# Kernel optimization log

Hardware: AMD Instinct MI355X
Metric: run time of the kernel (lower is better)

The kernel has to match this reference:

```python
import jax, jax.numpy as jnp
import numpy as np

N_MODELS = 16
IN_F = 1024
OUT_F = 1024
N_TOK = 8192


def setup_inputs() -> dict:
    key = jax.random.key(0)
    k1, k2, k3, k4 = jax.random.split(key, 4)
    x = jax.random.normal(k1, (N_TOK, IN_F), dtype=jnp.float32)
    idxs = jax.random.randint(k2, (N_TOK,), 0, N_MODELS, dtype=jnp.int64)
    w = jax.random.normal(k3, (N_MODELS, IN_F, OUT_F), dtype=jnp.float32) * 0.02
    b = jax.random.normal(k4, (N_MODELS, OUT_F), dtype=jnp.float32) * 0.02
    return {"x": x, "idxs": idxs, "w": w, "b": b}


def reference(x, idxs, w, b):
    # Equivalent math to the torch loop: for each expert i, tokens with
    # idxs==i get x @ w[i] + b[i]; finally ReLU over all outputs.
    # Loop over the small fixed expert count; selection by mask avoids
    # materializing the [N, E, out] tensor or gathering per-token weights.
    y = jnp.zeros((x.shape[0], w.shape[2]), dtype=x.dtype)
    for i in range(w.shape[0]):
        yi = x @ w[i] + b[i]  # [N, out]
        y = jnp.where((idxs == i)[:, None], yi, y)
    return jax.nn.relu(y)
```

## Files before the change

### kernel.cpp

```cpp
#include <hip/hip_runtime.h>
#include <hip/hip_bf16.h>
#include <stdint.h>

#define N_MODELS 16
#define IN_F 1024
#define OUT_F 1024
#define N_TOK 8192
#define MAX_MT 80

typedef unsigned short u16;
using us4   = __attribute__((ext_vector_type(4))) unsigned short;
using s16x8 = __attribute__((ext_vector_type(8))) short;
using f32x4 = __attribute__((ext_vector_type(4))) float;

__device__ __forceinline__ u16 f2bf(float f) {
    union { float f; uint32_t u; } v;
    v.f = f;
    uint32_t u = v.u;
    u += 0x7fffu + ((u >> 16) & 1u);
    return (u16)(u >> 16);
}

__device__ __forceinline__ void gload16(const u16* g, u16* l) {
    __builtin_amdgcn_global_load_lds(
        (const __attribute__((address_space(1))) void*)g,
        (__attribute__((address_space(3))) void*)l, 16, 0, 0);
}

__global__ void hist_kernel(const int* __restrict__ idxs, int* __restrict__ ghist) {
    __shared__ int cnt[N_MODELS];
    int t = threadIdx.x;
    if (t < N_MODELS) cnt[t] = 0;
    __syncthreads();
    int i = blockIdx.x * 256 + t;
    atomicAdd(&cnt[idxs[i]], 1);
    __syncthreads();
    if (t < N_MODELS) atomicAdd(&ghist[t], cnt[t]);
}

__global__ void scan_kernel(const int* __restrict__ ghist,
                            int* __restrict__ offs, int* __restrict__ tile_off,
                            int* __restrict__ gcur) {
    if (threadIdx.x == 0) {
        int o = 0, to = 0;
        for (int e = 0; e < N_MODELS; ++e) {
            offs[e] = o; tile_off[e] = to; gcur[e] = o;
            to += (ghist[e] + 127) >> 7;
            o  += ghist[e];
        }
        offs[N_MODELS] = o; tile_off[N_MODELS] = to;
    }
}

__global__ void scatter_kernel(const int* __restrict__ idxs,
                               int* __restrict__ gcur, int* __restrict__ perm) {
    int i = blockIdx.x * 256 + threadIdx.x;
    int e = idxs[i];
    int p = atomicAdd(&gcur[e], 1);
    perm[p] = i;
}

__global__ __launch_bounds__(256)
void wprep_kernel(const float* __restrict__ w, u16* __restrict__ wT) {
    int bx  = blockIdx.x;
    int e   = bx >> 7;
    int nt  = (bx >> 4) & 7;
    int kb2 = bx & 15;
    const float* wp = w + (size_t)e * (IN_F * OUT_F) + (size_t)kb2 * 64 * OUT_F + nt * 128;
    u16* ob = wT + ((size_t)(e * 8 + nt) * 32 + kb2 * 2) * 4096;
    int n    = threadIdx.x & 127;
    int half = threadIdx.x >> 7;
#pragma unroll
    for (int i = 0; i < 4; ++i) {
        int ko = half + i * 2;
        s16x8 v;
#pragma unroll
        for (int j = 0; j < 8; ++j)
            v[j] = (short)f2bf(wp[(size_t)(ko * 8 + j) * OUT_F + n]);
        *(s16x8*)(ob + ((size_t)((ko >> 2) * 4 + (ko & 3)) * 128 + n) * 8) = v;
    }
}

__global__ __launch_bounds__(256)
void xprep_kernel(const float* __restrict__ x,
                  const int* __restrict__ perm, const int* __restrict__ offs,
                  const int* __restrict__ tile_off, u16* __restrict__ xg) {
    __shared__ u16 sh[4096];
    int t   = threadIdx.x;
    int bx2 = blockIdx.x;
    int mt  = bx2 >> 3;
    int kg  = bx2 & 7;
    int total = tile_off[N_MODELS];
    if (mt >= total) return;
    int e = 0;
    while (tile_off[e + 1] <= mt) ++e;
    int s0   = offs[e] + (mt - tile_off[e]) * 128;
    int sEnd = offs[e + 1];
    int r0   = t >> 3;
    int apos = t & 7;
    int toks[4];
#pragma unroll
    for (int i = 0; i < 4; ++i) {
        int r = r0 + i * 32;
        toks[i] = (s0 + r < sEnd) ? perm[s0 + r] : -1;
    }
    u16* outx = xg + (size_t)mt * 32 * 4096;
    for (int kb4 = 0; kb4 < 4; ++kb4) {
        int kb = kg * 4 + kb4;
#pragma unroll
        for (int i = 0; i < 4; ++i) {
            int r = r0 + i * 32;
            int k = kb * 32 + apos * 4;
            float4 v;
            if (toks[i] >= 0) v = *(const float4*)(x + (size_t)toks[i] * IN_F + k);
            else              v = make_float4(0.f, 0.f, 0.f, 0.f);
            us4 pk; pk.x = f2bf(v.x); pk.y = f2bf(v.y); pk.z = f2bf(v.z); pk.w = f2bf(v.w);
            *(us4*)(&sh[(apos >> 1) * 1024 + r * 8 + (apos & 1) * 4]) = pk;
        }
        __syncthreads();
#pragma unroll
        for (int i = 0; i < 2; ++i) {
            int c = t + i * 256;
            *(s16x8*)(outx + (size_t)kb * 4096 + c * 8) = *(const s16x8*)(&sh[c * 8]);
        }
        __syncthreads();
    }
}

__global__ __launch_bounds__(256)
void gemm_kernel(const u16* __restrict__ xg, const u16* __restrict__ wT,
                 const float* __restrict__ bias,
                 const int* __restrict__ perm, const int* __restrict__ offs,
                 const int* __restrict__ tile_off,
                 float* __restrict__ out)
{
    __shared__ u16 As[4096];
    __shared__ u16 Bs[4096];
    __shared__ int   permS[128];
    __shared__ float biasS[128];
    __shared__ int   toS[N_MODELS + 1];

    int t  = threadIdx.x;
    int bt = blockIdx.y;
    int nt = blockIdx.x;

    if (t <= N_MODELS) toS[t] = tile_off[t];
    __syncthreads();
    if (bt >= toS[N_MODELS]) return;

    int e = 0;
    while (toS[e + 1] <= bt) ++e;
    int s0   = offs[e] + (bt - toS[e]) * 128;
    int sEnd = offs[e + 1];
    int mValid = sEnd - s0; if (mValid > 128) mValid = 128;

    if (t < 128) {
        permS[t] = (s0 + t < sEnd) ? perm[s0 + t] : 0;
        biasS[t] = bias[(size_t)e * OUT_F + nt * 128 + t];
    }

    const u16* atile = xg + (size_t)bt * 32 * 4096;
    const u16* btile = wT + ((size_t)(e * 8 + nt) * 32) * 4096;

    int lane = t & 63;
    int wv   = t >> 6;
    int wm   = (wv >> 1) * 64;
    int wn   = (wv & 1) * 64;
    int m    = lane & 15;
    int q    = lane >> 4;

    f32x4 acc[4][4];
#pragma unroll
    for (int i = 0; i < 4; ++i)
#pragma unroll
        for (int j = 0; j < 4; ++j)
            acc[i][j] = (f32x4){0.f, 0.f, 0.f, 0.f};

    int c = wv * 2;

    for (int kb = 0; kb < 32; ++kb) {
        const u16* ga = atile + kb * 4096;
        const u16* gb = btile + kb * 4096;
        gload16(ga + (c    ) * 512 + lane * 8, &As[(c    ) * 512]);
        gload16(ga + (c + 1) * 512 + lane * 8, &As[(c + 1) * 512]);
        gload16(gb + (c    ) * 512 + lane * 8, &Bs[(c    ) * 512]);
        gload16(gb + (c + 1) * 512 + lane * 8, &Bs[(c + 1) * 512]);
        __syncthreads();

        s16x8 af[4], bf[4];
#pragma unroll
        for (int mt2 = 0; mt2 < 4; ++mt2)
            af[mt2] = *(const s16x8*)(&As[q * 1024 + (wm + mt2 * 16 + m) * 8]);
#pragma unroll
        for (int nt2 = 0; nt2 < 4; ++nt2)
            bf[nt2] = *(const s16x8*)(&Bs[q * 1024 + (wn + nt2 * 16 + m) * 8]);
#pragma unroll
        for (int mt2 = 0; mt2 < 4; ++mt2)
#pragma unroll
            for (int nt2 = 0; nt2 < 4; ++nt2)
                acc[mt2][nt2] = __builtin_amdgcn_mfma_f32_16x16x32_bf16(
                    af[mt2], bf[nt2], acc[mt2][nt2], 0, 0, 0);
        __syncthreads();
    }

#pragma unroll
    for (int mt2 = 0; mt2 < 4; ++mt2) {
        int rbase = wm + mt2 * 16 + q * 4;
#pragma unroll
        for (int i = 0; i < 4; ++i) {
            int r = rbase + i;
            if (r < mValid) {
                int tok = permS[r];
                float* orow = out + (size_t)tok * OUT_F + nt * 128;
#pragma unroll
                for (int nt2 = 0; nt2 < 4; ++nt2) {
                    int col = wn + nt2 * 16 + m;
                    float v = acc[mt2][nt2][i] + biasS[col];
                    orow[col] = v > 0.f ? v : 0.f;
                }
            }
        }
    }
}

extern "C" void kernel_launch(void* const* d_in, const int* in_sizes, int n_in,
                              void* d_out, int out_size, void* d_ws, size_t ws_size,
                              hipStream_t stream) {
    const float* x    = (const float*)d_in[0];
    const int*   idxs = (const int*)d_in[1];
    const float* w    = (const float*)d_in[2];
    const float* b    = (const float*)d_in[3];
    float* out = (float*)d_out;

    u16* wT = (u16*)d_ws;
    u16* xg = wT + (size_t)N_MODELS * IN_F * OUT_F;
    int* perm     = (int*)(xg + (size_t)MAX_MT * 32 * 4096);
    int* offs     = perm + N_TOK;
    int* tile_off = offs + (N_MODELS + 1);
    int* ghist    = tile_off + (N_MODELS + 1);
    int* gcur     = ghist + N_MODELS;

    hipMemsetAsync(ghist, 0, N_MODELS * sizeof(int), stream);
    hist_kernel<<<N_TOK / 256, 256, 0, stream>>>(idxs, ghist);
    scan_kernel<<<1, 64, 0, stream>>>(ghist, offs, tile_off, gcur);
    scatter_kernel<<<N_TOK / 256, 256, 0, stream>>>(idxs, gcur, perm);
    wprep_kernel<<<16 * 8 * 16, 256, 0, stream>>>(w, wT);
    xprep_kernel<<<MAX_MT * 8, 256, 0, stream>>>(x, perm, offs, tile_off, xg);
    gemm_kernel<<<dim3(8, MAX_MT), 256, 0, stream>>>(xg, wT, b, perm, offs, tile_off, out);
}
```

Before: 212.0 us.

## Fuse routing setup into one block and merge weight/activation prep kernels

```diff
diff --git a/kernel.cpp b/kernel.cpp
--- a/kernel.cpp
+++ b/kernel.cpp
@@ -27,103 +27,142 @@
         (__attribute__((address_space(3))) void*)l, 16, 0, 0);
 }
 
-__global__ void hist_kernel(const int* __restrict__ idxs, int* __restrict__ ghist) {
-    __shared__ int cnt[N_MODELS];
+#define ROW 17
+__global__ __launch_bounds__(256)
+void setup_kernel(const int* __restrict__ idxs,
+                  int* __restrict__ perm,
+                  int* __restrict__ offs,
+                  int* __restrict__ tile_off)
+{
+    __shared__ int cnt[256 * ROW];
+    __shared__ int offsS[N_MODELS + 1];
     int t = threadIdx.x;
-    if (t < N_MODELS) cnt[t] = 0;
-    __syncthreads();
-    int i = blockIdx.x * 256 + t;
-    atomicAdd(&cnt[idxs[i]], 1);
-    __syncthreads();
-    if (t < N_MODELS) atomicAdd(&ghist[t], cnt[t]);
-}
-
-__global__ void scan_kernel(const int* __restrict__ ghist,
-                            int* __restrict__ offs, int* __restrict__ tile_off,
-                            int* __restrict__ gcur) {
-    if (threadIdx.x == 0) {
+
+#pragma unroll
+    for (int e = 0; e < N_MODELS; ++e) cnt[t * ROW + e] = 0;
+    __syncthreads();
+
+    int base = t * 32;
+#pragma unroll
+    for (int i = 0; i < 32; ++i) {
+        int e = idxs[base + i];
+        cnt[t * ROW + e] += 1;
+    }
+    __syncthreads();
+
+#pragma unroll
+    for (int s = 1; s < 256; s <<= 1) {
+        int v[N_MODELS];
+#pragma unroll
+        for (int e = 0; e < N_MODELS; ++e)
+            v[e] = (t >= s) ? cnt[(t - s) * ROW + e] : 0;
+        __syncthreads();
+#pragma unroll
+        for (int e = 0; e < N_MODELS; ++e)
+            cnt[t * ROW + e] += v[e];
+        __syncthreads();
+    }
+
+    if (t == 0) {
         int o = 0, to = 0;
         for (int e = 0; e < N_MODELS; ++e) {
-            offs[e] = o; tile_off[e] = to; gcur[e] = o;
-            to += (ghist[e] + 127) >> 7;
-            o  += ghist[e];
-        }
+            int c = cnt[255 * ROW + e];
+            offsS[e] = o;
+            offs[e] = o; tile_off[e] = to;
+            to += (c + 127) >> 7;
+            o  += c;
+        }
+        offsS[N_MODELS] = o;
         offs[N_MODELS] = o; tile_off[N_MODELS] = to;
     }
-}
-
-__global__ void scatter_kernel(const int* __restrict__ idxs,
-                               int* __restrict__ gcur, int* __restrict__ perm) {
-    int i = blockIdx.x * 256 + threadIdx.x;
-    int e = idxs[i];
-    int p = atomicAdd(&gcur[e], 1);
-    perm[p] = i;
-}
+    __syncthreads();
+
+    int cur[N_MODELS];
+#pragma unroll
+    for (int e = 0; e < N_MODELS; ++e)
+        cur[e] = offsS[e] + ((t > 0) ? cnt[(t - 1) * ROW + e] : 0);
+    __syncthreads();
+#pragma unroll
+    for (int e = 0; e < N_MODELS; ++e) cnt[t * ROW + e] = cur[e];
+
+#pragma unroll
+    for (int i = 0; i < 32; ++i) {
+        int tok = base + i;
+        int e = idxs[tok];
+        int p = cnt[t * ROW + e]++;
+        perm[p] = tok;
+    }
+}
+
+#define WBLOCKS (16 * 8 * 16)
+#define XBLOCKS (MAX_MT * 8)
 
 __global__ __launch_bounds__(256)
-void wprep_kernel(const float* __restrict__ w, u16* __restrict__ wT) {
-    int bx  = blockIdx.x;
-    int e   = bx >> 7;
-    int nt  = (bx >> 4) & 7;
-    int kb2 = bx & 15;
-    const float* wp = w + (size_t)e * (IN_F * OUT_F) + (size_t)kb2 * 64 * OUT_F + nt * 128;
-    u16* ob = wT + ((size_t)(e * 8 + nt) * 32 + kb2 * 2) * 4096;
-    int n    = threadIdx.x & 127;
-    int half = threadIdx.x >> 7;
-#pragma unroll
-    for (int i = 0; i < 4; ++i) {
-        int ko = half + i * 2;
-        s16x8 v;
-#pragma unroll
-        for (int j = 0; j < 8; ++j)
-            v[j] = (short)f2bf(wp[(size_t)(ko * 8 + j) * OUT_F + n]);
-        *(s16x8*)(ob + ((size_t)((ko >> 2) * 4 + (ko & 3)) * 128 + n) * 8) = v;
-    }
-}
-
-__global__ __launch_bounds__(256)
-void xprep_kernel(const float* __restrict__ x,
-                  const int* __restrict__ perm, const int* __restrict__ offs,
-                  const int* __restrict__ tile_off, u16* __restrict__ xg) {
-    __shared__ u16 sh[4096];
-    int t   = threadIdx.x;
-    int bx2 = blockIdx.x;
-    int mt  = bx2 >> 3;
-    int kg  = bx2 & 7;
-    int total = tile_off[N_MODELS];
-    if (mt >= total) return;
-    int e = 0;
-    while (tile_off[e + 1] <= mt) ++e;
-    int s0   = offs[e] + (mt - tile_off[e]) * 128;
-    int sEnd = offs[e + 1];
-    int r0   = t >> 3;
-    int apos = t & 7;
-    int toks[4];
-#pragma unroll
-    for (int i = 0; i < 4; ++i) {
-        int r = r0 + i * 32;
-        toks[i] = (s0 + r < sEnd) ? perm[s0 + r] : -1;
-    }
-    u16* outx = xg + (size_t)mt * 32 * 4096;
-    for (int kb4 = 0; kb4 < 4; ++kb4) {
-        int kb = kg * 4 + kb4;
+void prep_kernel(const float* __restrict__ w, const float* __restrict__ x,
+                 const int* __restrict__ perm, const int* __restrict__ offs,
+                 const int* __restrict__ tile_off,
+                 u16* __restrict__ wT, u16* __restrict__ xg)
+{
+    int t  = threadIdx.x;
+    int bx = blockIdx.x;
+
+    if (bx < WBLOCKS) {
+        int e   = bx >> 7;
+        int nt  = (bx >> 4) & 7;
+        int kb2 = bx & 15;
+        const float* wp = w + (size_t)e * (IN_F * OUT_F) + (size_t)kb2 * 64 * OUT_F + nt * 128;
+        u16* ob = wT + ((size_t)(e * 8 + nt) * 32 + kb2 * 2) * 4096;
+        int n    = t & 127;
+        int half = t >> 7;
+#pragma unroll
+        for (int i = 0; i < 4; ++i) {
+            int ko = half + i * 2;
+            s16x8 v;
+#pragma unroll
+            for (int j = 0; j < 8; ++j)
+                v[j] = (short)f2bf(wp[(size_t)(ko * 8 + j) * OUT_F + n]);
+            *(s16x8*)(ob + ((size_t)((ko >> 2) * 4 + (ko & 3)) * 128 + n) * 8) = v;
+        }
+    } else {
+        __shared__ u16 sh[4096];
+        int bx2 = bx - WBLOCKS;
+        int mt  = bx2 >> 3;
+        int kg  = bx2 & 7;
+        int total = tile_off[N_MODELS];
+        if (mt >= total) return;
+        int e = 0;
+        while (tile_off[e + 1] <= mt) ++e;
+        int s0   = offs[e] + (mt - tile_off[e]) * 128;
+        int sEnd = offs[e + 1];
+        int r0   = t >> 3;
+        int apos = t & 7;
+        int toks[4];
 #pragma unroll
         for (int i = 0; i < 4; ++i) {
             int r = r0 + i * 32;
-            int k = kb * 32 + apos * 4;
-            float4 v;
-            if (toks[i] >= 0) v = *(const float4*)(x + (size_t)toks[i] * IN_F + k);
-            else              v = make_float4(0.f, 0.f, 0.f, 0.f);
-            us4 pk; pk.x = f2bf(v.x); pk.y = f2bf(v.y); pk.z = f2bf(v.z); pk.w = f2bf(v.w);
-            *(us4*)(&sh[(apos >> 1) * 1024 + r * 8 + (apos & 1) * 4]) = pk;
-        }
-        __syncthreads();
-#pragma unroll
-        for (int i = 0; i < 2; ++i) {
-            int c = t + i * 256;
-            *(s16x8*)(outx + (size_t)kb * 4096 + c * 8) = *(const s16x8*)(&sh[c * 8]);
-        }
-        __syncthreads();
+            toks[i] = (s0 + r < sEnd) ? perm[s0 + r] : -1;
+        }
+        u16* outx = xg + (size_t)mt * 32 * 4096;
+        for (int kb4 = 0; kb4 < 4; ++kb4) {
+            int kb = kg * 4 + kb4;
+#pragma unroll
+            for (int i = 0; i < 4; ++i) {
+                int r = r0 + i * 32;
+                int k = kb * 32 + apos * 4;
+                float4 v;
+                if (toks[i] >= 0) v = *(const float4*)(x + (size_t)toks[i] * IN_F + k);
+                else              v = make_float4(0.f, 0.f, 0.f, 0.f);
+                us4 pk; pk.x = f2bf(v.x); pk.y = f2bf(v.y); pk.z = f2bf(v.z); pk.w = f2bf(v.w);
+                *(us4*)(&sh[(apos >> 1) * 1024 + r * 8 + (apos & 1) * 4]) = pk;
+            }
+            __syncthreads();
+#pragma unroll
+            for (int i = 0; i < 2; ++i) {
+                int c = t + i * 256;
+                *(s16x8*)(outx + (size_t)kb * 4096 + c * 8) = *(const s16x8*)(&sh[c * 8]);
+            }
+            __syncthreads();
+        }
     }
 }
 
@@ -237,14 +276,8 @@
     int* perm     = (int*)(xg + (size_t)MAX_MT * 32 * 4096);
     int* offs     = perm + N_TOK;
     int* tile_off = offs + (N_MODELS + 1);
-    int* ghist    = tile_off + (N_MODELS + 1);
-    int* gcur     = ghist + N_MODELS;
-
-    hipMemsetAsync(ghist, 0, N_MODELS * sizeof(int), stream);
-    hist_kernel<<<N_TOK / 256, 256, 0, stream>>>(idxs, ghist);
-    scan_kernel<<<1, 64, 0, stream>>>(ghist, offs, tile_off, gcur);
-    scatter_kernel<<<N_TOK / 256, 256, 0, stream>>>(idxs, gcur, perm);
-    wprep_kernel<<<16 * 8 * 16, 256, 0, stream>>>(w, wT);
-    xprep_kernel<<<MAX_MT * 8, 256, 0, stream>>>(x, perm, offs, tile_off, xg);
+
+    setup_kernel<<<1, 256, 0, stream>>>(idxs, perm, offs, tile_off);
+    prep_kernel<<<WBLOCKS + XBLOCKS, 256, 0, stream>>>(w, x, perm, offs, tile_off, wT, xg);
     gemm_kernel<<<dim3(8, MAX_MT), 256, 0, stream>>>(xg, wT, b, perm, offs, tile_off, out);
 }
```

Result: faster. 186.3 us (-12.1%).
